# Kernel optimization log

Measured on AMD Instinct MI355X. Metric: run time of the kernel, lower is better.

## Reference

```python
import jax, jax.numpy as jnp
import numpy as np

D_MODEL = 512
NUM_HEADS = 8
D_HEAD = D_MODEL // NUM_HEADS


def setup_inputs() -> dict:
    key = jax.random.key(0)
    ks = jax.random.split(key, 9)
    B, L = 4, 2048
    s = 1.0 / np.sqrt(D_MODEL)
    inp = {
        "x": jax.random.normal(ks[0], (B, L, D_MODEL), dtype=jnp.float32),
        "Wq": jax.random.uniform(ks[1], (D_MODEL, D_MODEL), jnp.float32, -s, s),
        "bq": jax.random.uniform(ks[2], (D_MODEL,), jnp.float32, -s, s),
        "Wk": jax.random.uniform(ks[3], (D_MODEL, D_MODEL), jnp.float32, -s, s),
        "bk": jax.random.uniform(ks[4], (D_MODEL,), jnp.float32, -s, s),
        "Wv": jax.random.uniform(ks[5], (D_MODEL, D_MODEL), jnp.float32, -s, s),
        "bv": jax.random.uniform(ks[6], (D_MODEL,), jnp.float32, -s, s),
        "Wo": jax.random.uniform(ks[7], (D_MODEL, D_MODEL), jnp.float32, -s, s),
        "bo": jax.random.uniform(ks[8], (D_MODEL,), jnp.float32, -s, s),
    }
    return inp


def reference(x, Wq, bq, Wk, bk, Wv, bv, Wo, bo):
    B, L, _ = x.shape
    def split_heads(t):  # [B,L,D] -> [B,H,L,d]
        return t.reshape(B, L, NUM_HEADS, D_HEAD).transpose(0, 2, 1, 3)
    Q = split_heads(x @ Wq + bq)
    K = split_heads(x @ Wk + bk)
    V = split_heads(x @ Wv + bv)
    scale = 1.0 / jnp.sqrt(jnp.asarray(D_HEAD, dtype=x.dtype))
    scores = jnp.einsum('bhqd,bhkd->bhqk', Q, K) * scale  # [B,H,L,L]
    weights = jax.nn.softmax(scores, axis=-1)
    z = jnp.einsum('bhqk,bhkd->bhqd', weights, V)  # [B,H,L,d]
    z = z.transpose(0, 2, 1, 3).reshape(B, L, D_MODEL)
    return z @ Wo + bo
```

## Files before the change

### kernel.cpp

```cpp
#include <hip/hip_runtime.h>
#include <hip/hip_bf16.h>
#include <math.h>


#define MDIM 8192
#define DMODEL 512
#define NHEAD 8
#define DHEAD 64
#define LSEQ 2048

typedef __attribute__((ext_vector_type(8))) short short8;
typedef __attribute__((ext_vector_type(4))) float floatx4;

struct alignas(16) bf16x8 { __hip_bfloat16 v[8]; };
struct alignas(8)  bf16x4 { __hip_bfloat16 v[4]; };

__device__ __forceinline__ void load_lds16(const __hip_bfloat16* g, __hip_bfloat16* l) {
    __builtin_amdgcn_global_load_lds(
        (const __attribute__((address_space(1))) void*)g,
        (__attribute__((address_space(3))) void*)l,
        16, 0, 0);
}

__device__ __forceinline__ float fast_exp2(float x) {
#if __has_builtin(__builtin_amdgcn_exp2f)
    return __builtin_amdgcn_exp2f(x);
#else
    return __expf(x * 0.69314718055994531f);
#endif
}

__global__ __launch_bounds__(256) void cast_x_kernel(
    const float* __restrict__ x, __hip_bfloat16* __restrict__ xb)
{
    size_t i = ((size_t)blockIdx.x * 256 + threadIdx.x) * 8;
    float4 a = *reinterpret_cast<const float4*>(x + i);
    float4 b = *reinterpret_cast<const float4*>(x + i + 4);
    bf16x8 o;
    o.v[0] = __float2bfloat16(a.x); o.v[1] = __float2bfloat16(a.y);
    o.v[2] = __float2bfloat16(a.z); o.v[3] = __float2bfloat16(a.w);
    o.v[4] = __float2bfloat16(b.x); o.v[5] = __float2bfloat16(b.y);
    o.v[6] = __float2bfloat16(b.z); o.v[7] = __float2bfloat16(b.w);
    *reinterpret_cast<bf16x8*>(xb + i) = o;
}

__global__ __launch_bounds__(256) void transpose_cast_w(
    const float* __restrict__ Wq, const float* __restrict__ Wk,
    const float* __restrict__ Wv, const float* __restrict__ Wo,
    __hip_bfloat16* __restrict__ Wt)
{
    __shared__ float t[32][33];
    const int z = blockIdx.z;
    const float* W = z == 0 ? Wq : (z == 1 ? Wk : (z == 2 ? Wv : Wo));
    __hip_bfloat16* dst = Wt + ((size_t)z << 18);
    int k0 = blockIdx.x * 32, n0 = blockIdx.y * 32;
    int c = threadIdx.x & 31, r = threadIdx.x >> 5;
    #pragma unroll
    for (int i = 0; i < 4; ++i)
        t[r + 8 * i][c] = W[(size_t)(k0 + r + 8 * i) * DMODEL + n0 + c];
    __syncthreads();
    #pragma unroll
    for (int i = 0; i < 4; ++i)
        dst[(size_t)(n0 + r + 8 * i) * DMODEL + k0 + c] = __float2bfloat16(t[c][r + 8 * i]);
}

__global__ __launch_bounds__(256) void gemm_qkv_mfma(
    const __hip_bfloat16* __restrict__ xb,
    const __hip_bfloat16* __restrict__ Wt,
    const float* __restrict__ bq, const float* __restrict__ bk,
    const float* __restrict__ bv,
    __hip_bfloat16* __restrict__ Q, __hip_bfloat16* __restrict__ K,
    __hip_bfloat16* __restrict__ Vt)
{
    __shared__ __hip_bfloat16 As[128 * 64];
    __shared__ __hip_bfloat16 Bs[128 * 64];

    const int tid = threadIdx.x;
    const int wid = tid >> 6, lane = tid & 63;
    const int l16 = lane & 15, quad = lane >> 4;
    const int wr = wid >> 1, wc = wid & 1;
    const int row0 = blockIdx.x * 128;
    const int which = blockIdx.y >> 2;
    const int col0 = (blockIdx.y & 3) * 128;
    const __hip_bfloat16* Wb = Wt + ((size_t)which << 18);
    const float* bias = which == 0 ? bq : (which == 1 ? bk : bv);

    const int r8 = lane >> 3, slot = lane & 7;
    const int cchunk = slot ^ (r8 & 7);

    floatx4 acc[4][4];
    #pragma unroll
    for (int i = 0; i < 4; ++i)
        #pragma unroll
        for (int j = 0; j < 4; ++j) acc[i][j] = floatx4{0.f, 0.f, 0.f, 0.f};

    for (int kt = 0; kt < DMODEL / 64; ++kt) {
        __syncthreads();
        #pragma unroll
        for (int j = 0; j < 4; ++j) {
            int seg = wid * 4 + j;
            int m = seg * 8 + r8;
            load_lds16(xb + (size_t)(row0 + m) * DMODEL + kt * 64 + cchunk * 8,
                       As + seg * 512);
            load_lds16(Wb + (size_t)(col0 + m) * DMODEL + kt * 64 + cchunk * 8,
                       Bs + seg * 512);
        }
        __syncthreads();

        #pragma unroll
        for (int ks = 0; ks < 2; ++ks) {
            const int c = ks * 4 + quad;
            short8 af[4], bf[4];
            #pragma unroll
            for (int mt = 0; mt < 4; ++mt) {
                int m = wr * 64 + mt * 16 + l16;
                af[mt] = *reinterpret_cast<const short8*>(As + m * 64 + ((c ^ (m & 7)) << 3));
            }
            #pragma unroll
            for (int nt = 0; nt < 4; ++nt) {
                int n = wc * 64 + nt * 16 + l16;
                bf[nt] = *reinterpret_cast<const short8*>(Bs + n * 64 + ((c ^ (n & 7)) << 3));
            }
            #pragma unroll
            for (int mt = 0; mt < 4; ++mt)
                #pragma unroll
                for (int nt = 0; nt < 4; ++nt)
                    acc[mt][nt] = __builtin_amdgcn_mfma_f32_16x16x32_bf16(
                        af[mt], bf[nt], acc[mt][nt], 0, 0, 0);
        }
    }

    const float QSCALE = 0.18033688011112042f;
    #pragma unroll
    for (int mt = 0; mt < 4; ++mt) {
        const int mmbase = row0 + wr * 64 + mt * 16 + quad * 4;
        const int b = mmbase >> 11;
        const int l = mmbase & 2047;
        #pragma unroll
        for (int nt = 0; nt < 4; ++nt) {
            const int nn = col0 + wc * 64 + nt * 16 + l16;
            const float bias_v = bias[nn];
            const int h = nn >> 6, dd = nn & 63;
            const int bh = b * NHEAD + h;
            if (which == 2) {
                bf16x4 pk;
                #pragma unroll
                for (int r = 0; r < 4; ++r)
                    pk.v[r] = __float2bfloat16(acc[mt][nt][r] + bias_v);
                *reinterpret_cast<bf16x4*>(Vt + ((size_t)bh * DHEAD + dd) * LSEQ + l) = pk;
            } else if (which == 0) {
                #pragma unroll
                for (int r = 0; r < 4; ++r)
                    Q[(((size_t)bh * LSEQ + l + r) << 6) + dd] =
                        __float2bfloat16((acc[mt][nt][r] + bias_v) * QSCALE);
            } else {
                #pragma unroll
                for (int r = 0; r < 4; ++r)
                    K[(((size_t)bh * LSEQ + l + r) << 6) + dd] =
                        __float2bfloat16(acc[mt][nt][r] + bias_v);
            }
        }
    }
}

__global__ __launch_bounds__(256) void gemm_out_mfma(
    const __hip_bfloat16* __restrict__ Zb,
    const __hip_bfloat16* __restrict__ WoT,
    const float* __restrict__ bo, float* __restrict__ out)
{
    __shared__ __hip_bfloat16 As[128 * 64];
    __shared__ __hip_bfloat16 Bs[128 * 64];

    const int tid = threadIdx.x;
    const int wid = tid >> 6, lane = tid & 63;
    const int l16 = lane & 15, quad = lane >> 4;
    const int wr = wid >> 1, wc = wid & 1;
    const int row0 = blockIdx.x * 128;
    const int col0 = blockIdx.y * 128;
    const int r8 = lane >> 3, slot = lane & 7;
    const int cchunk = slot ^ (r8 & 7);

    floatx4 acc[4][4];
    #pragma unroll
    for (int i = 0; i < 4; ++i)
        #pragma unroll
        for (int j = 0; j < 4; ++j) acc[i][j] = floatx4{0.f, 0.f, 0.f, 0.f};

    for (int kt = 0; kt < DMODEL / 64; ++kt) {
        __syncthreads();
        #pragma unroll
        for (int j = 0; j < 4; ++j) {
            int seg = wid * 4 + j;
            int m = seg * 8 + r8;
            load_lds16(Zb + (size_t)(row0 + m) * DMODEL + kt * 64 + cchunk * 8,
                       As + seg * 512);
            load_lds16(WoT + (size_t)(col0 + m) * DMODEL + kt * 64 + cchunk * 8,
                       Bs + seg * 512);
        }
        __syncthreads();

        #pragma unroll
        for (int ks = 0; ks < 2; ++ks) {
            const int c = ks * 4 + quad;
            short8 af[4], bf[4];
            #pragma unroll
            for (int mt = 0; mt < 4; ++mt) {
                int m = wr * 64 + mt * 16 + l16;
                af[mt] = *reinterpret_cast<const short8*>(As + m * 64 + ((c ^ (m & 7)) << 3));
            }
            #pragma unroll
            for (int nt = 0; nt < 4; ++nt) {
                int n = wc * 64 + nt * 16 + l16;
                bf[nt] = *reinterpret_cast<const short8*>(Bs + n * 64 + ((c ^ (n & 7)) << 3));
            }
            #pragma unroll
            for (int mt = 0; mt < 4; ++mt)
                #pragma unroll
                for (int nt = 0; nt < 4; ++nt)
                    acc[mt][nt] = __builtin_amdgcn_mfma_f32_16x16x32_bf16(
                        af[mt], bf[nt], acc[mt][nt], 0, 0, 0);
        }
    }

    #pragma unroll
    for (int mt = 0; mt < 4; ++mt) {
        const int mmbase = row0 + wr * 64 + mt * 16 + quad * 4;
        #pragma unroll
        for (int nt = 0; nt < 4; ++nt) {
            const int nn = col0 + wc * 64 + nt * 16 + l16;
            const float bias_v = bo[nn];
            #pragma unroll
            for (int r = 0; r < 4; ++r)
                out[(size_t)(mmbase + r) * DMODEL + nn] = acc[mt][nt][r] + bias_v;
        }
    }
}

__global__ __launch_bounds__(256) void attn_mfma(
    const __hip_bfloat16* __restrict__ Q,
    const __hip_bfloat16* __restrict__ K,
    const __hip_bfloat16* __restrict__ Vt,
    __hip_bfloat16* __restrict__ Z)
{
    __shared__ __align__(16) char smem[40960];
    __hip_bfloat16* Qs = (__hip_bfloat16*)smem;
    __hip_bfloat16* Ks = (__hip_bfloat16*)(smem + 8192);
    __hip_bfloat16* Vs = (__hip_bfloat16*)(smem + 24576);

    const int bh = blockIdx.x >> 5;
    const int q0 = (blockIdx.x & 31) * 64;
    const int tid = threadIdx.x;
    const int wid = tid >> 6, lane = tid & 63;
    const int l16 = lane & 15, quad = lane >> 4;
    const int r8 = lane >> 3, slot = lane & 7;
    const int cchunk = slot ^ (r8 & 7);

    const __hip_bfloat16* Qg = Q + ((size_t)bh * LSEQ + q0) * DHEAD;
    const __hip_bfloat16* Kg = K + (size_t)bh * LSEQ * DHEAD;
    const __hip_bfloat16* Vg = Vt + (size_t)bh * DHEAD * LSEQ;

    #pragma unroll
    for (int j = 0; j < 2; ++j) {
        int seg = wid * 2 + j;
        int m = seg * 8 + r8;
        load_lds16(Qg + ((size_t)m << 6) + cchunk * 8, Qs + seg * 512);
    }
    __syncthreads();

    short8 qb[4][2];
    #pragma unroll
    for (int nt = 0; nt < 4; ++nt) {
        int q = nt * 16 + l16;
        #pragma unroll
        for (int s = 0; s < 2; ++s)
            qb[nt][s] = *reinterpret_cast<const short8*>(
                Qs + q * 64 + (((s * 4 + quad) ^ (q & 7)) << 3));
    }

    floatx4 acc[4][4];
    #pragma unroll
    for (int i = 0; i < 4; ++i)
        #pragma unroll
        for (int j = 0; j < 4; ++j) acc[i][j] = floatx4{0.f, 0.f, 0.f, 0.f};
    float lsum[4] = {0.f, 0.f, 0.f, 0.f};

    for (int kt = 0; kt < LSEQ / 128; ++kt) {
        __syncthreads();
        #pragma unroll
        for (int j = 0; j < 4; ++j) {
            int seg = wid * 4 + j;
            int rho = seg * 8 + r8;
            int g = (rho & 96) | (((rho >> 2) & 3) << 3) | (((rho >> 4) & 1) << 2) | (rho & 3);
            load_lds16(Kg + ((size_t)(kt * 128 + g) << 6) + cchunk * 8, Ks + seg * 512);
            int d = seg * 4 + (lane >> 4);
            int gch = (lane & 15) ^ (d & 7);
            load_lds16(Vg + (size_t)d * LSEQ + kt * 128 + gch * 8, Vs + seg * 512);
        }
        __syncthreads();

        floatx4 sacc[2][4];
        #pragma unroll
        for (int t = 0; t < 2; ++t)
            #pragma unroll
            for (int nt = 0; nt < 4; ++nt) sacc[t][nt] = floatx4{0.f, 0.f, 0.f, 0.f};
        #pragma unroll
        for (int s = 0; s < 2; ++s) {
            const int swz = ((s * 4 + quad) ^ (l16 & 7)) << 3;
            short8 kb0 = *reinterpret_cast<const short8*>(Ks + (wid * 32 + l16) * 64 + swz);
            short8 kb1 = *reinterpret_cast<const short8*>(Ks + (wid * 32 + 16 + l16) * 64 + swz);
            #pragma unroll
            for (int nt = 0; nt < 4; ++nt) {
                sacc[0][nt] = __builtin_amdgcn_mfma_f32_16x16x32_bf16(kb0, qb[nt][s], sacc[0][nt], 0, 0, 0);
                sacc[1][nt] = __builtin_amdgcn_mfma_f32_16x16x32_bf16(kb1, qb[nt][s], sacc[1][nt], 0, 0, 0);
            }
        }

        short8 pa[4];
        #pragma unroll
        for (int nt = 0; nt < 4; ++nt) {
            union { short8 s8; __hip_bfloat16 h[8]; } u;
            #pragma unroll
            for (int t = 0; t < 2; ++t)
                #pragma unroll
                for (int r = 0; r < 4; ++r) {
                    float p = fast_exp2(sacc[t][nt][r]);
                    lsum[nt] += p;
                    u.h[t * 4 + r] = __float2bfloat16(p);
                }
            pa[nt] = u.s8;
        }

        #pragma unroll
        for (int dt = 0; dt < 4; ++dt) {
            short8 vb = *reinterpret_cast<const short8*>(
                Vs + (dt * 16 + l16) * 128 + (((wid * 4 + quad) ^ (l16 & 7)) << 3));
            #pragma unroll
            for (int nt = 0; nt < 4; ++nt)
                acc[nt][dt] = __builtin_amdgcn_mfma_f32_16x16x32_bf16(pa[nt], vb, acc[nt][dt], 0, 0, 0);
        }
    }

    __syncthreads();
    float* Lred = (float*)smem;
    float* Ored = (float*)(smem + 8192);

    #pragma unroll
    for (int nt = 0; nt < 4; ++nt) {
        float v = lsum[nt];
        v += __shfl_xor(v, 16);
        v += __shfl_xor(v, 32);
        lsum[nt] = v;
    }
    if (quad == 0) {
        #pragma unroll
        for (int nt = 0; nt < 4; ++nt)
            Lred[wid * 64 + nt * 16 + l16] = lsum[nt];
    }

    const int b = bh >> 3, h = bh & 7;
    const int ql = tid >> 2;
    const int dg = tid & 3;
    float inv = 0.f;

    for (int dt = 0; dt < 4; ++dt) {
        __syncthreads();
        #pragma unroll
        for (int nt = 0; nt < 4; ++nt)
            *reinterpret_cast<floatx4*>(
                &Ored[(wid * 16 + l16) * 68 + nt * 16 + quad * 4]) = acc[nt][dt];
        __syncthreads();

        if (dt == 0)
            inv = 1.f / (Lred[ql] + Lred[64 + ql] + Lred[128 + ql] + Lred[192 + ql]);

        bf16x4 zo;
        #pragma unroll
        for (int i = 0; i < 4; ++i) {
            int d = dg * 4 + i;
            float ssum = Ored[d * 68 + ql] + Ored[(16 + d) * 68 + ql]
                       + Ored[(32 + d) * 68 + ql] + Ored[(48 + d) * 68 + ql];
            zo.v[i] = __float2bfloat16(ssum * inv);
        }
        *reinterpret_cast<bf16x4*>(
            Z + (size_t)(b * LSEQ + q0 + ql) * DMODEL + h * 64 + dt * 16 + dg * 4) = zo;
    }
}

extern "C" void kernel_launch(void* const* d_in, const int* in_sizes, int n_in,
                              void* d_out, int out_size, void* d_ws, size_t ws_size,
                              hipStream_t stream)
{
    const float* x  = (const float*)d_in[0];
    const float* Wq = (const float*)d_in[1]; const float* bq = (const float*)d_in[2];
    const float* Wk = (const float*)d_in[3]; const float* bk = (const float*)d_in[4];
    const float* Wv = (const float*)d_in[5]; const float* bv = (const float*)d_in[6];
    const float* Wo = (const float*)d_in[7]; const float* bo = (const float*)d_in[8];
    float* out = (float*)d_out;

    const size_t nqkv = (size_t)MDIM * DMODEL;
    __hip_bfloat16* xb = (__hip_bfloat16*)d_ws;
    __hip_bfloat16* Wt = xb + nqkv;
    __hip_bfloat16* Qb = Wt + ((size_t)4 << 18);
    __hip_bfloat16* Kb = Qb + nqkv;
    __hip_bfloat16* Vb = Kb + nqkv;
    __hip_bfloat16* Zb = Vb + nqkv;

    cast_x_kernel<<<dim3(MDIM * DMODEL / (256 * 8)), 256, 0, stream>>>(x, xb);
    transpose_cast_w<<<dim3(16, 16, 4), 256, 0, stream>>>(Wq, Wk, Wv, Wo, Wt);

    gemm_qkv_mfma<<<dim3(MDIM / 128, 12), 256, 0, stream>>>(
        xb, Wt, bq, bk, bv, Qb, Kb, Vb);

    attn_mfma<<<dim3(32 * (LSEQ / 64)), 256, 0, stream>>>(Qb, Kb, Vb, Zb);

    gemm_out_mfma<<<dim3(MDIM / 128, DMODEL / 128), 256, 0, stream>>>(
        Zb, Wt + ((size_t)3 << 18), bo, out);
}
```

Measured before the change: 177.5 us.

## Store Q/K/V in MFMA fragment order and load attention operands directly from global

The QKV projection now writes Q, K and V into a pre-swizzled, fragment-major layout (with K rows permuted and the MFMA operand order swapped for Q/K), so each lane can read its MFMA operand as one contiguous 16-byte load. The attention kernel drops LDS staging and all per-tile __syncthreads, reading K/V fragments straight from global memory into registers. Block indexing is also reordered so consecutive blocks share the same head, improving L2 reuse of K/V. Each wave now fetches K/V independently from global/L2 rather than sharing a block-wide LDS copy, and with no prefetch, load latency may be exposed.

```diff
diff --git a/kernel.cpp b/kernel.cpp
--- a/kernel.cpp
+++ b/kernel.cpp
@@ -69,8 +69,8 @@
     const __hip_bfloat16* __restrict__ Wt,
     const float* __restrict__ bq, const float* __restrict__ bk,
     const float* __restrict__ bv,
-    __hip_bfloat16* __restrict__ Q, __hip_bfloat16* __restrict__ K,
-    __hip_bfloat16* __restrict__ Vt)
+    __hip_bfloat16* __restrict__ Q2, __hip_bfloat16* __restrict__ K2,
+    __hip_bfloat16* __restrict__ V2)
 {
     __shared__ __hip_bfloat16 As[128 * 64];
     __shared__ __hip_bfloat16 Bs[128 * 64];
@@ -121,43 +121,80 @@
                 int n = wc * 64 + nt * 16 + l16;
                 bf[nt] = *reinterpret_cast<const short8*>(Bs + n * 64 + ((c ^ (n & 7)) << 3));
             }
-            #pragma unroll
-            for (int mt = 0; mt < 4; ++mt)
+            if (which < 2) {
                 #pragma unroll
-                for (int nt = 0; nt < 4; ++nt)
-                    acc[mt][nt] = __builtin_amdgcn_mfma_f32_16x16x32_bf16(
-                        af[mt], bf[nt], acc[mt][nt], 0, 0, 0);
+                for (int mt = 0; mt < 4; ++mt)
+                    #pragma unroll
+                    for (int nt = 0; nt < 4; ++nt)
+                        acc[mt][nt] = __builtin_amdgcn_mfma_f32_16x16x32_bf16(
+                            bf[nt], af[mt], acc[mt][nt], 0, 0, 0);
+            } else {
+                #pragma unroll
+                for (int mt = 0; mt < 4; ++mt)
+                    #pragma unroll
+                    for (int nt = 0; nt < 4; ++nt)
+                        acc[mt][nt] = __builtin_amdgcn_mfma_f32_16x16x32_bf16(
+                            af[mt], bf[nt], acc[mt][nt], 0, 0, 0);
+            }
         }
     }
 
     const float QSCALE = 0.18033688011112042f;
-    #pragma unroll
-    for (int mt = 0; mt < 4; ++mt) {
-        const int mmbase = row0 + wr * 64 + mt * 16 + quad * 4;
-        const int b = mmbase >> 11;
-        const int l = mmbase & 2047;
-        #pragma unroll
-        for (int nt = 0; nt < 4; ++nt) {
-            const int nn = col0 + wc * 64 + nt * 16 + l16;
-            const float bias_v = bias[nn];
-            const int h = nn >> 6, dd = nn & 63;
-            const int bh = b * NHEAD + h;
-            if (which == 2) {
+
+    if (which < 2) {
+        __hip_bfloat16* dst = (which == 0) ? Q2 : K2;
+        #pragma unroll
+        for (int mt = 0; mt < 4; ++mt) {
+            const int mm = row0 + wr * 64 + mt * 16 + l16;
+            const int b = mm >> 11, l = mm & 2047;
+            int rowi;
+            if (which == 0) {
+                rowi = l;
+            } else {
+                int hi = l & ~127, w7 = l & 127;
+                rowi = hi | (w7 & 96) | (((w7 >> 3) & 3) << 2)
+                          | (((w7 >> 2) & 1) << 4) | (w7 & 3);
+            }
+            #pragma unroll
+            for (int nt = 0; nt < 4; ++nt) {
+                const int nnb = col0 + wc * 64 + nt * 16 + quad * 4;
+                const float4 bv4 = *reinterpret_cast<const float4*>(&bias[nnb]);
+                const int h = nnb >> 6, d = nnb & 63;
+                const int s = d >> 5, q4 = (d >> 3) & 3, jb = d & 7;
+                bf16x4 pk;
+                if (which == 0) {
+                    pk.v[0] = __float2bfloat16((acc[mt][nt][0] + bv4.x) * QSCALE);
+                    pk.v[1] = __float2bfloat16((acc[mt][nt][1] + bv4.y) * QSCALE);
+                    pk.v[2] = __float2bfloat16((acc[mt][nt][2] + bv4.z) * QSCALE);
+                    pk.v[3] = __float2bfloat16((acc[mt][nt][3] + bv4.w) * QSCALE);
+                } else {
+                    pk.v[0] = __float2bfloat16(acc[mt][nt][0] + bv4.x);
+                    pk.v[1] = __float2bfloat16(acc[mt][nt][1] + bv4.y);
+                    pk.v[2] = __float2bfloat16(acc[mt][nt][2] + bv4.z);
+                    pk.v[3] = __float2bfloat16(acc[mt][nt][3] + bv4.w);
+                }
+                size_t idx = ((((size_t)(b * NHEAD + h) * 128 + (rowi >> 4)) * 2 + s) << 9)
+                             + q4 * 128 + (rowi & 15) * 8 + jb;
+                *reinterpret_cast<bf16x4*>(dst + idx) = pk;
+            }
+        }
+    } else {
+        #pragma unroll
+        for (int mt = 0; mt < 4; ++mt) {
+            const int mmb = row0 + wr * 64 + mt * 16 + quad * 4;
+            const int b = mmb >> 11, lb = mmb & 2047;
+            #pragma unroll
+            for (int nt = 0; nt < 4; ++nt) {
+                const int nn = col0 + wc * 64 + nt * 16 + l16;
+                const int h = nn >> 6, d = nn & 63;
+                const float bv = bias[nn];
                 bf16x4 pk;
                 #pragma unroll
                 for (int r = 0; r < 4; ++r)
-                    pk.v[r] = __float2bfloat16(acc[mt][nt][r] + bias_v);
-                *reinterpret_cast<bf16x4*>(Vt + ((size_t)bh * DHEAD + dd) * LSEQ + l) = pk;
-            } else if (which == 0) {
-                #pragma unroll
-                for (int r = 0; r < 4; ++r)
-                    Q[(((size_t)bh * LSEQ + l + r) << 6) + dd] =
-                        __float2bfloat16((acc[mt][nt][r] + bias_v) * QSCALE);
-            } else {
-                #pragma unroll
-                for (int r = 0; r < 4; ++r)
-                    K[(((size_t)bh * LSEQ + l + r) << 6) + dd] =
-                        __float2bfloat16(acc[mt][nt][r] + bias_v);
+                    pk.v[r] = __float2bfloat16(acc[mt][nt][r] + bv);
+                size_t idx = ((((size_t)(b * NHEAD + h) * 64 + (lb >> 5)) * 4 + (d >> 4)) << 9)
+                             + ((lb >> 3) & 3) * 128 + (d & 15) * 8 + (lb & 7);
+                *reinterpret_cast<bf16x4*>(V2 + idx) = pk;
             }
         }
     }
@@ -237,45 +274,32 @@
 }
 
 __global__ __launch_bounds__(256) void attn_mfma(
-    const __hip_bfloat16* __restrict__ Q,
-    const __hip_bfloat16* __restrict__ K,
-    const __hip_bfloat16* __restrict__ Vt,
+    const __hip_bfloat16* __restrict__ Q2,
+    const __hip_bfloat16* __restrict__ K2,
+    const __hip_bfloat16* __restrict__ V2,
     __hip_bfloat16* __restrict__ Z)
 {
-    __shared__ __align__(16) char smem[40960];
-    __hip_bfloat16* Qs = (__hip_bfloat16*)smem;
-    __hip_bfloat16* Ks = (__hip_bfloat16*)(smem + 8192);
-    __hip_bfloat16* Vs = (__hip_bfloat16*)(smem + 24576);
-
-    const int bh = blockIdx.x >> 5;
-    const int q0 = (blockIdx.x & 31) * 64;
+    __shared__ float smem[4608];
+    float* Lred = smem;
+    float* Ored = smem + 256;
+
+    const int bh = blockIdx.x & 31;
+    const int qt = blockIdx.x >> 5;
+    const int q0 = qt * 64;
     const int tid = threadIdx.x;
     const int wid = tid >> 6, lane = tid & 63;
     const int l16 = lane & 15, quad = lane >> 4;
-    const int r8 = lane >> 3, slot = lane & 7;
-    const int cchunk = slot ^ (r8 & 7);
-
-    const __hip_bfloat16* Qg = Q + ((size_t)bh * LSEQ + q0) * DHEAD;
-    const __hip_bfloat16* Kg = K + (size_t)bh * LSEQ * DHEAD;
-    const __hip_bfloat16* Vg = Vt + (size_t)bh * DHEAD * LSEQ;
-
-    #pragma unroll
-    for (int j = 0; j < 2; ++j) {
-        int seg = wid * 2 + j;
-        int m = seg * 8 + r8;
-        load_lds16(Qg + ((size_t)m << 6) + cchunk * 8, Qs + seg * 512);
-    }
-    __syncthreads();
+
+    const __hip_bfloat16* Kc = K2 + (((size_t)bh * 128 * 2) << 9);
+    const __hip_bfloat16* Vc = V2 + (((size_t)bh * 64 * 4) << 9);
 
     short8 qb[4][2];
     #pragma unroll
-    for (int nt = 0; nt < 4; ++nt) {
-        int q = nt * 16 + l16;
+    for (int nt = 0; nt < 4; ++nt)
         #pragma unroll
         for (int s = 0; s < 2; ++s)
             qb[nt][s] = *reinterpret_cast<const short8*>(
-                Qs + q * 64 + (((s * 4 + quad) ^ (q & 7)) << 3));
-    }
+                Q2 + ((((size_t)bh * 128 + qt * 4 + nt) * 2 + s) << 9) + lane * 8);
 
     floatx4 acc[4][4];
     #pragma unroll
@@ -285,18 +309,17 @@
     float lsum[4] = {0.f, 0.f, 0.f, 0.f};
 
     for (int kt = 0; kt < LSEQ / 128; ++kt) {
-        __syncthreads();
-        #pragma unroll
-        for (int j = 0; j < 4; ++j) {
-            int seg = wid * 4 + j;
-            int rho = seg * 8 + r8;
-            int g = (rho & 96) | (((rho >> 2) & 3) << 3) | (((rho >> 4) & 1) << 2) | (rho & 3);
-            load_lds16(Kg + ((size_t)(kt * 128 + g) << 6) + cchunk * 8, Ks + seg * 512);
-            int d = seg * 4 + (lane >> 4);
-            int gch = (lane & 15) ^ (d & 7);
-            load_lds16(Vg + (size_t)d * LSEQ + kt * 128 + gch * 8, Vs + seg * 512);
-        }
-        __syncthreads();
+        short8 kb[2][2], vb[4];
+        #pragma unroll
+        for (int t = 0; t < 2; ++t)
+            #pragma unroll
+            for (int s = 0; s < 2; ++s)
+                kb[t][s] = *reinterpret_cast<const short8*>(
+                    Kc + ((((size_t)(kt * 8 + wid * 2 + t)) * 2 + s) << 9) + lane * 8);
+        #pragma unroll
+        for (int dt = 0; dt < 4; ++dt)
+            vb[dt] = *reinterpret_cast<const short8*>(
+                Vc + ((((size_t)(kt * 4 + wid)) * 4 + dt) << 9) + lane * 8);
 
         floatx4 sacc[2][4];
         #pragma unroll
@@ -305,13 +328,12 @@
             for (int nt = 0; nt < 4; ++nt) sacc[t][nt] = floatx4{0.f, 0.f, 0.f, 0.f};
         #pragma unroll
         for (int s = 0; s < 2; ++s) {
-            const int swz = ((s * 4 + quad) ^ (l16 & 7)) << 3;
-            short8 kb0 = *reinterpret_cast<const short8*>(Ks + (wid * 32 + l16) * 64 + swz);
-            short8 kb1 = *reinterpret_cast<const short8*>(Ks + (wid * 32 + 16 + l16) * 64 + swz);
             #pragma unroll
             for (int nt = 0; nt < 4; ++nt) {
-                sacc[0][nt] = __builtin_amdgcn_mfma_f32_16x16x32_bf16(kb0, qb[nt][s], sacc[0][nt], 0, 0, 0);
-                sacc[1][nt] = __builtin_amdgcn_mfma_f32_16x16x32_bf16(kb1, qb[nt][s], sacc[1][nt], 0, 0, 0);
+                sacc[0][nt] = __builtin_amdgcn_mfma_f32_16x16x32_bf16(
+                    kb[0][s], qb[nt][s], sacc[0][nt], 0, 0, 0);
+                sacc[1][nt] = __builtin_amdgcn_mfma_f32_16x16x32_bf16(
+                    kb[1][s], qb[nt][s], sacc[1][nt], 0, 0, 0);
             }
         }
 
@@ -331,18 +353,12 @@
         }
 
         #pragma unroll
-        for (int dt = 0; dt < 4; ++dt) {
-            short8 vb = *reinterpret_cast<const short8*>(
-                Vs + (dt * 16 + l16) * 128 + (((wid * 4 + quad) ^ (l16 & 7)) << 3));
+        for (int dt = 0; dt < 4; ++dt)
             #pragma unroll
             for (int nt = 0; nt < 4; ++nt)
-                acc[nt][dt] = __builtin_amdgcn_mfma_f32_16x16x32_bf16(pa[nt], vb, acc[nt][dt], 0, 0, 0);
-        }
-    }
-
-    __syncthreads();
-    float* Lred = (float*)smem;
-    float* Ored = (float*)(smem + 8192);
+                acc[nt][dt] = __builtin_amdgcn_mfma_f32_16x16x32_bf16(
+                    pa[nt], vb[dt], acc[nt][dt], 0, 0, 0);
+    }
 
     #pragma unroll
     for (int nt = 0; nt < 4; ++nt) {
@@ -400,18 +416,18 @@
     const size_t nqkv = (size_t)MDIM * DMODEL;
     __hip_bfloat16* xb = (__hip_bfloat16*)d_ws;
     __hip_bfloat16* Wt = xb + nqkv;
-    __hip_bfloat16* Qb = Wt + ((size_t)4 << 18);
-    __hip_bfloat16* Kb = Qb + nqkv;
-    __hip_bfloat16* Vb = Kb + nqkv;
-    __hip_bfloat16* Zb = Vb + nqkv;
+    __hip_bfloat16* Q2 = Wt + ((size_t)4 << 18);
+    __hip_bfloat16* K2 = Q2 + nqkv;
+    __hip_bfloat16* V2 = K2 + nqkv;
+    __hip_bfloat16* Zb = V2 + nqkv;
 
     cast_x_kernel<<<dim3(MDIM * DMODEL / (256 * 8)), 256, 0, stream>>>(x, xb);
     transpose_cast_w<<<dim3(16, 16, 4), 256, 0, stream>>>(Wq, Wk, Wv, Wo, Wt);
 
     gemm_qkv_mfma<<<dim3(MDIM / 128, 12), 256, 0, stream>>>(
-        xb, Wt, bq, bk, bv, Qb, Kb, Vb);
-
-    attn_mfma<<<dim3(32 * (LSEQ / 64)), 256, 0, stream>>>(Qb, Kb, Vb, Zb);
+        xb, Wt, bq, bk, bv, Q2, K2, V2);
+
+    attn_mfma<<<dim3(32 * (LSEQ / 64)), 256, 0, stream>>>(Q2, K2, V2, Zb);
 
     gemm_out_mfma<<<dim3(MDIM / 128, DMODEL / 128), 256, 0, stream>>>(
         Zb, Wt + ((size_t)3 << 18), bo, out);
```

Result: faster. 162.2 us (-8.6%).
